# Kernel tuning notes

Measured on AMD Instinct MI355X. Metric: run time of the kernel, lower is better.

Reference implementation:

```python
import jax, jax.numpy as jnp
import numpy as np

B, L, DM = 4, 4096, 1024
DK, DV = 128, 128


def setup_inputs() -> dict:
    key = jax.random.key(0)
    kq, kk, kv, kwq, kwk, kwv = jax.random.split(key, 6)
    scale = 1.0 / np.sqrt(DM)
    return {
        "Q": jax.random.normal(kq, (B, L, DM), dtype=jnp.float32),
        "K": jax.random.normal(kk, (B, L, DM), dtype=jnp.float32),
        "V": jax.random.normal(kv, (B, L, DM), dtype=jnp.float32),
        "mask": jnp.ones((B, 1, L), dtype=jnp.int32),
        "WQ": jax.random.normal(kwq, (DM, DK), dtype=jnp.float32) * scale,
        "WK": jax.random.normal(kwk, (DM, DK), dtype=jnp.float32) * scale,
        "WV": jax.random.normal(kwv, (DM, DV), dtype=jnp.float32) * scale,
    }


def reference(Q, K, V, mask, WQ, WK, WV):
    # Projections (Dense, no bias): [B, L, dm] @ [dm, dk/dv]
    q = jnp.einsum("bld,dk->blk", Q, WQ)  # [B, L, dk]
    k = jnp.einsum("bld,dk->blk", K, WK)  # [B, L, dk]
    v = jnp.einsum("bld,dv->blv", V, WV)  # [B, L, dv]
    # Raw scores [B, L, L]
    qk = jnp.einsum("bqk,bsk->bqs", q, k)
    # Faithful to original: mask applied BEFORE scaling by 1/sqrt(dk)
    qk = jnp.where(mask == 1, qk, -jnp.inf)
    qk = qk / jnp.sqrt(jnp.asarray(DK, dtype=qk.dtype))
    attn = jax.nn.softmax(qk, axis=-1)
    return jnp.einsum("bqs,bsv->bqv", attn, v)  # [B, L, dv]
```

## Files before the change

### kernel.cpp

```cpp
#include <hip/hip_runtime.h>
#include <hip/hip_bf16.h>

#define B_  4
#define L_  4096
#define DM_ 1024
#define DK_ 128
#define DV_ 128
#define KS_ 4
#define ROWS_ (B_ * L_)

typedef __bf16 bf16x8 __attribute__((ext_vector_type(8)));
typedef float  f32x4  __attribute__((ext_vector_type(4)));

__device__ __forceinline__ void dma16(const void* g, void* l) {
    __builtin_amdgcn_global_load_lds(
        (const __attribute__((address_space(1))) void*)g,
        (__attribute__((address_space(3))) void*)l, 16, 0, 0);
}

#define WAITBAR0() __asm__ volatile("s_waitcnt vmcnt(0) lgkmcnt(0)\ns_barrier" ::: "memory")

__device__ __forceinline__ float rowmax_dpp(float v) {
    int x;
    x = __float_as_int(v);
    v = fmaxf(v, __int_as_float(__builtin_amdgcn_update_dpp(x, x, 0x121, 0xF, 0xF, false)));
    x = __float_as_int(v);
    v = fmaxf(v, __int_as_float(__builtin_amdgcn_update_dpp(x, x, 0x122, 0xF, 0xF, false)));
    x = __float_as_int(v);
    v = fmaxf(v, __int_as_float(__builtin_amdgcn_update_dpp(x, x, 0x124, 0xF, 0xF, false)));
    x = __float_as_int(v);
    v = fmaxf(v, __int_as_float(__builtin_amdgcn_update_dpp(x, x, 0x128, 0xF, 0xF, false)));
    return v;
}

__global__ __launch_bounds__(256) void wt_kernel(
    const float* __restrict__ WQ, const float* __restrict__ WK,
    const float* __restrict__ WV, __bf16* __restrict__ WT)
{
    const int mat = blockIdx.y;
    const float* W = (mat == 0) ? WQ : (mat == 1) ? WK : WV;
    const float scl = (mat == 0) ? 0.088388347648318447f : 1.0f;
    __bf16* Wt = WT + (size_t)mat * DK_ * DM_;

    __shared__ float lds[DK_][33];
    const int t  = threadIdx.x;
    const int d0 = blockIdx.x * 32;

    for (int i = 0; i < 16; ++i) {
        int idx = i * 256 + t;
        int dd = idx >> 7, n = idx & 127;
        lds[n][dd] = W[(size_t)(d0 + dd) * DK_ + n] * scl;
    }
    __syncthreads();
    for (int i = 0; i < 16; ++i) {
        int idx = i * 256 + t;
        int n = idx >> 5, dd = idx & 31;
        Wt[(size_t)n * DM_ + d0 + dd] = (__bf16)lds[n][dd];
    }
}

__global__ __launch_bounds__(256, 4) void proj_kernel(
    const float* __restrict__ Q, const float* __restrict__ K, const float* __restrict__ V,
    const __bf16* __restrict__ WT,
    __bf16* __restrict__ qb, __bf16* __restrict__ kb, __bf16* __restrict__ vT)
{
    const int mat = blockIdx.y;
    const float* X = (mat == 0) ? Q : (mat == 1) ? K : V;
    const __bf16* Wt = WT + (size_t)mat * DK_ * DM_;

    __shared__ __bf16 wbuf[2][128 * 64];

    const int t    = threadIdx.x;
    const int w    = t >> 6;
    const int l    = t & 63;
    const int quad = l >> 4;
    const int c16  = l & 15;
    const int m0   = blockIdx.x * 64 + w * 16;
    const float* xrow = &X[(size_t)(m0 + c16) * DM_];

    const __bf16* wg[4];
    for (int i = 0; i < 4; ++i) {
        int row = (w * 4 + i) * 8 + (l >> 3);
        int lc  = (l & 7) ^ (row & 7);
        wg[i] = Wt + (size_t)row * DM_ + lc * 8;
    }

    f32x4 acc[8];
    for (int i = 0; i < 8; ++i) acc[i] = {0.f, 0.f, 0.f, 0.f};

    for (int i = 0; i < 4; ++i)
        dma16(wg[i], &wbuf[0][(w * 4 + i) * 512]);
    float4 xn[4];
    for (int dd = 0; dd < 2; ++dd)
        for (int p = 0; p < 2; ++p)
            xn[dd * 2 + p] = *(const float4*)(xrow + dd * 32 + quad * 8 + p * 4);
    WAITBAR0();

    for (int kt = 0; kt < 16; ++kt) {
        const int cur = kt & 1, nxt = cur ^ 1;
        float4 xc[4];
        for (int i = 0; i < 4; ++i) xc[i] = xn[i];
        if (kt < 15) {
            const int d1 = (kt + 1) * 64;
            for (int i = 0; i < 4; ++i)
                dma16(wg[i] + d1, &wbuf[nxt][(w * 4 + i) * 512]);
            for (int dd = 0; dd < 2; ++dd)
                for (int p = 0; p < 2; ++p)
                    xn[dd * 2 + p] = *(const float4*)(xrow + d1 + dd * 32 + quad * 8 + p * 4);
        }

        for (int dd = 0; dd < 2; ++dd) {
            float4 x0 = xc[dd * 2], x1 = xc[dd * 2 + 1];
            bf16x8 af;
            af[0] = (__bf16)x0.x; af[1] = (__bf16)x0.y; af[2] = (__bf16)x0.z; af[3] = (__bf16)x0.w;
            af[4] = (__bf16)x1.x; af[5] = (__bf16)x1.y; af[6] = (__bf16)x1.z; af[7] = (__bf16)x1.w;
            for (int nt = 0; nt < 8; ++nt) {
                bf16x8 bfv = *(const bf16x8*)
                    &wbuf[cur][(nt * 16 + c16) * 64 + (((dd * 4 + quad) ^ (c16 & 7)) << 3)];
                acc[nt] = __builtin_amdgcn_mfma_f32_16x16x32_bf16(af, bfv, acc[nt], 0, 0, 0);
            }
        }
        if (kt < 15) WAITBAR0();
    }

    if (mat < 2) {
        __bf16* outp = (mat == 0) ? qb : kb;
        for (int nt = 0; nt < 8; ++nt)
            for (int r = 0; r < 4; ++r)
                outp[(size_t)(m0 + quad * 4 + r) * DK_ + nt * 16 + c16] = (__bf16)acc[nt][r];
    } else {
        for (int nt = 0; nt < 8; ++nt)
            for (int r = 0; r < 4; ++r) {
                int row = m0 + quad * 4 + r;
                int b = row >> 12, s = row & (L_ - 1);
                vT[((size_t)b * DV_ + nt * 16 + c16) * L_ + s] = (__bf16)acc[nt][r];
            }
    }
}

__global__ __launch_bounds__(256, 2) void attn_kernel(
    const __bf16* __restrict__ qb, const __bf16* __restrict__ kb,
    const __bf16* __restrict__ vT, const int* __restrict__ mask,
    __bf16* __restrict__ ob_part, float* __restrict__ ml_part)
{
    __shared__ __bf16 kbuf[2][64 * 128];
    __shared__ __bf16 vbuf[2][128 * 64];
    __shared__ __bf16 p_lds[4][16 * 76];

    const int t    = threadIdx.x;
    const int w    = t >> 6;
    const int l    = t & 63;
    const int quad = l >> 4;
    const int c16  = l & 15;

    const int combo = blockIdx.x & 15;
    const int b     = combo & 3;
    const int ks    = combo >> 2;
    const int qt    = blockIdx.x >> 4;
    const int m0    = qt * 64 + w * 16;
    const size_t bL = (size_t)b * L_;
    const int kbase = ks * (L_ / KS_);

    const __bf16* kg[4];
    const __bf16* vg[4];
    for (int i = 0; i < 4; ++i) {
        int kr  = (w * 4 + i) * 4 + (l >> 4);
        int klc = (l & 15) ^ (kr & 15);
        kg[i] = kb + (bL + kbase + kr) * DK_ + klc * 8;
        int vr  = (w * 4 + i) * 8 + (l >> 3);
        int vlc = (l & 7) ^ (vr & 7);
        vg[i] = vT + ((size_t)b * DV_ + vr) * L_ + kbase + vlc * 8;
    }

    bf16x8 qf[4];
    {
        const __bf16* qrow = &qb[(bL + m0 + c16) * DK_];
        for (int dt = 0; dt < 4; ++dt)
            qf[dt] = *(const bf16x8*)&qrow[dt * 32 + quad * 8];
    }

    unsigned int mbits = 0;
    for (int g = 0; g < 4; ++g) {
        const int4 mv = *(const int4*)&mask[bL + kbase + g * 256 + l * 4];
        bool ok = (mv.x == 1) && (mv.y == 1) && (mv.z == 1) && (mv.w == 1);
        unsigned long long bm = __ballot(ok);
        for (int cc = 0; cc < 4; ++cc)
            if (((bm >> (16 * cc)) & 0xFFFFull) == 0xFFFFull)
                mbits |= 1u << (g * 4 + cc);
    }

    bf16x8 onesv;
    for (int i = 0; i < 8; ++i) onesv[i] = (__bf16)1.0f;

    f32x4 o[8], osum;
    for (int i = 0; i < 8; ++i) o[i] = {0.f, 0.f, 0.f, 0.f};
    osum = {0.f, 0.f, 0.f, 0.f};
    float mst[4];
    for (int r = 0; r < 4; ++r) mst[r] = -1e30f;

    for (int i = 0; i < 4; ++i) dma16(kg[i], &kbuf[0][(w * 4 + i) * 512]);
    for (int i = 0; i < 4; ++i) dma16(vg[i], &vbuf[0][(w * 4 + i) * 512]);
    WAITBAR0();

    for (int sc = 0; sc < (L_ / KS_) / 64; ++sc) {
        const int cur = sc & 1, nxt = cur ^ 1;
        if (sc < 15) {
            for (int i = 0; i < 4; ++i)
                dma16(kg[i] + (size_t)(sc + 1) * 64 * DK_, &kbuf[nxt][(w * 4 + i) * 512]);
            for (int i = 0; i < 4; ++i)
                dma16(vg[i] + (sc + 1) * 64, &vbuf[nxt][(w * 4 + i) * 512]);
        }

        f32x4 sacc[4];
        for (int nt = 0; nt < 4; ++nt) sacc[nt] = {0.f, 0.f, 0.f, 0.f};
        for (int dt = 0; dt < 4; ++dt)
            for (int nt = 0; nt < 4; ++nt) {
                bf16x8 kf = *(const bf16x8*)
                    &kbuf[cur][(nt * 16 + c16) * 128 + (((dt * 4 + quad) ^ c16) << 3)];
                sacc[nt] = __builtin_amdgcn_mfma_f32_16x16x32_bf16(qf[dt], kf, sacc[nt], 0, 0, 0);
            }

        if (!((mbits >> sc) & 1)) {
            const int s0 = kbase + sc * 64;
            for (int nt = 0; nt < 4; ++nt) {
                int mk = mask[bL + s0 + nt * 16 + c16];
                for (int r = 0; r < 4; ++r)
                    if (mk != 1) sacc[nt][r] = -1e30f;
            }
        }

        float nm[4];
        bool up = false;
        for (int r = 0; r < 4; ++r) {
            float cm = fmaxf(fmaxf(sacc[0][r], sacc[1][r]), fmaxf(sacc[2][r], sacc[3][r]));
            cm = rowmax_dpp(cm);
            nm[r] = fmaxf(mst[r], cm);
            up |= (nm[r] > mst[r]);
        }
        if (__ballot(up)) {
            float alpha[4];
            for (int r = 0; r < 4; ++r) {
                alpha[r] = __expf(mst[r] - nm[r]);
                mst[r] = nm[r];
            }
            for (int vt = 0; vt < 8; ++vt)
                for (int r = 0; r < 4; ++r) o[vt][r] *= alpha[r];
            for (int r = 0; r < 4; ++r) osum[r] *= alpha[r];
        }

        for (int r = 0; r < 4; ++r)
            for (int nt = 0; nt < 4; ++nt) {
                float p = __expf(sacc[nt][r] - nm[r]);
                p_lds[w][(quad * 4 + r) * 76 + nt * 16 + c16] = (__bf16)p;
            }
        __asm__ volatile("s_waitcnt lgkmcnt(0)" ::: "memory");

        for (int kt = 0; kt < 2; ++kt) {
            bf16x8 pf = *(const bf16x8*)&p_lds[w][c16 * 76 + kt * 32 + quad * 8];
            for (int vt = 0; vt < 8; ++vt) {
                bf16x8 vf = *(const bf16x8*)
                    &vbuf[cur][(vt * 16 + c16) * 64 + (((kt * 4 + quad) ^ (c16 & 7)) << 3)];
                o[vt] = __builtin_amdgcn_mfma_f32_16x16x32_bf16(pf, vf, o[vt], 0, 0, 0);
            }
            osum = __builtin_amdgcn_mfma_f32_16x16x32_bf16(pf, onesv, osum, 0, 0, 0);
        }

        if (sc < 15) WAITBAR0();
    }

    __bf16* op = ob_part + ((size_t)ks * ROWS_ + bL + m0) * DV_;
    for (int vt = 0; vt < 8; ++vt)
        for (int r = 0; r < 4; ++r)
            op[(size_t)(quad * 4 + r) * DV_ + vt * 16 + c16] = (__bf16)o[vt][r];
    if (c16 == 0)
        for (int r = 0; r < 4; ++r) {
            size_t row = (size_t)ks * ROWS_ + bL + m0 + quad * 4 + r;
            ml_part[row * 2 + 0] = mst[r];
            ml_part[row * 2 + 1] = osum[r];
        }
}

__global__ __launch_bounds__(256) void combine_kernel(
    const __bf16* __restrict__ ob_part, const float* __restrict__ ml_part,
    float* __restrict__ out)
{
    const int gid = blockIdx.x * 256 + threadIdx.x;
    const int row = gid >> 5;
    const int c4  = (gid & 31) << 2;

    float m[KS_], lv[KS_];
    float M = -1e30f;
    for (int s = 0; s < KS_; ++s) {
        m[s]  = ml_part[((size_t)s * ROWS_ + row) * 2 + 0];
        lv[s] = ml_part[((size_t)s * ROWS_ + row) * 2 + 1];
        M = fmaxf(M, m[s]);
    }
    float Lt = 0.f, acc[4] = {0.f, 0.f, 0.f, 0.f};
    for (int s = 0; s < KS_; ++s) {
        float ws = __expf(m[s] - M);
        Lt += lv[s] * ws;
        const __bf16* op = ob_part + ((size_t)s * ROWS_ + row) * DV_ + c4;
        for (int c = 0; c < 4; ++c) acc[c] += (float)op[c] * ws;
    }
    float rL = 1.0f / Lt;
    for (int c = 0; c < 4; ++c)
        out[(size_t)row * DV_ + c4 + c] = acc[c] * rL;
}

extern "C" void kernel_launch(void* const* d_in, const int* in_sizes, int n_in,
                              void* d_out, int out_size, void* d_ws, size_t ws_size,
                              hipStream_t stream) {
    const float* Q    = (const float*)d_in[0];
    const float* K    = (const float*)d_in[1];
    const float* V    = (const float*)d_in[2];
    const int*   mask = (const int*)d_in[3];
    const float* WQ   = (const float*)d_in[4];
    const float* WK   = (const float*)d_in[5];
    const float* WV   = (const float*)d_in[6];
    float* out = (float*)d_out;

    __bf16* qb = (__bf16*)d_ws;
    __bf16* kb = qb + (size_t)ROWS_ * DK_;
    __bf16* vT = kb + (size_t)ROWS_ * DK_;
    __bf16* WT = vT + (size_t)ROWS_ * DV_;
    __bf16* ob_part = WT + (size_t)3 * DK_ * DM_;
    float*  ml_part = (float*)(ob_part + (size_t)KS_ * ROWS_ * DV_);

    wt_kernel<<<dim3(DM_ / 32, 3), 256, 0, stream>>>(WQ, WK, WV, WT);
    proj_kernel<<<dim3(ROWS_ / 64, 3), 256, 0, stream>>>(Q, K, V, WT, qb, kb, vT);
    attn_kernel<<<dim3((ROWS_ / 64) * KS_), 256, 0, stream>>>(qb, kb, vT, mask, ob_part, ml_part);
    combine_kernel<<<dim3(ROWS_ * 32 / 256), 256, 0, stream>>>(ob_part, ml_part, out);
}
```

Measured before the change: 289.6 us.

## Load projection weights directly into registers instead of LDS double-buffering

The projection kernel drops the LDS staging buffer and the per-step barriers for the weight tile. Each lane now loads its bf16 weight fragments straight from global memory into registers, double-buffered at half-tile granularity. The X prefetch depth grows to two K-steps and the loop is fully unrolled. Every wave now re-reads the weight rows from global/L2, which raises register pressure, so the occupancy hint drops from 4 to 3 blocks.

New measurement: 344.3 us. 18.9% more time.

```diff
diff --git a/kernel.cpp b/kernel.cpp
--- a/kernel.cpp
+++ b/kernel.cpp
@@ -59,7 +59,7 @@
     }
 }
 
-__global__ __launch_bounds__(256, 4) void proj_kernel(
+__global__ __launch_bounds__(256, 3) void proj_kernel(
     const float* __restrict__ Q, const float* __restrict__ K, const float* __restrict__ V,
     const __bf16* __restrict__ WT,
     __bf16* __restrict__ qb, __bf16* __restrict__ kb, __bf16* __restrict__ vT)
@@ -68,8 +68,6 @@
     const float* X = (mat == 0) ? Q : (mat == 1) ? K : V;
     const __bf16* Wt = WT + (size_t)mat * DK_ * DM_;
 
-    __shared__ __bf16 wbuf[2][128 * 64];
-
     const int t    = threadIdx.x;
     const int w    = t >> 6;
     const int l    = t & 63;
@@ -78,49 +76,50 @@
     const int m0   = blockIdx.x * 64 + w * 16;
     const float* xrow = &X[(size_t)(m0 + c16) * DM_];
 
-    const __bf16* wg[4];
-    for (int i = 0; i < 4; ++i) {
-        int row = (w * 4 + i) * 8 + (l >> 3);
-        int lc  = (l & 7) ^ (row & 7);
-        wg[i] = Wt + (size_t)row * DM_ + lc * 8;
-    }
+    const __bf16* wp[8];
+    for (int nt = 0; nt < 8; ++nt)
+        wp[nt] = Wt + (size_t)(nt * 16 + c16) * DM_ + quad * 8;
 
     f32x4 acc[8];
     for (int i = 0; i < 8; ++i) acc[i] = {0.f, 0.f, 0.f, 0.f};
 
-    for (int i = 0; i < 4; ++i)
-        dma16(wg[i], &wbuf[0][(w * 4 + i) * 512]);
-    float4 xn[4];
-    for (int dd = 0; dd < 2; ++dd)
-        for (int p = 0; p < 2; ++p)
-            xn[dd * 2 + p] = *(const float4*)(xrow + dd * 32 + quad * 8 + p * 4);
-    WAITBAR0();
-
+    bf16x8 wf[2][8];
+    float4 xn[2][4];
+
+    for (int nt = 0; nt < 8; ++nt)
+        wf[0][nt] = *(const bf16x8*)(wp[nt]);
+    for (int c = 0; c < 2; ++c)
+        for (int dd = 0; dd < 2; ++dd)
+            for (int p = 0; p < 2; ++p)
+                xn[c][dd * 2 + p] = *(const float4*)(xrow + c * 64 + dd * 32 + quad * 8 + p * 4);
+
+#pragma unroll
     for (int kt = 0; kt < 16; ++kt) {
-        const int cur = kt & 1, nxt = cur ^ 1;
         float4 xc[4];
-        for (int i = 0; i < 4; ++i) xc[i] = xn[i];
-        if (kt < 15) {
-            const int d1 = (kt + 1) * 64;
-            for (int i = 0; i < 4; ++i)
-                dma16(wg[i] + d1, &wbuf[nxt][(w * 4 + i) * 512]);
+        for (int i = 0; i < 4; ++i) xc[i] = xn[kt & 1][i];
+        if (kt < 14) {
+            const int d2 = (kt + 2) * 64;
             for (int dd = 0; dd < 2; ++dd)
                 for (int p = 0; p < 2; ++p)
-                    xn[dd * 2 + p] = *(const float4*)(xrow + d1 + dd * 32 + quad * 8 + p * 4);
+                    xn[kt & 1][dd * 2 + p] = *(const float4*)(xrow + d2 + dd * 32 + quad * 8 + p * 4);
         }
 
         for (int dd = 0; dd < 2; ++dd) {
+            if (dd == 0) {
+                for (int nt = 0; nt < 8; ++nt)
+                    wf[1][nt] = *(const bf16x8*)(wp[nt] + kt * 64 + 32);
+            } else if (kt < 15) {
+                for (int nt = 0; nt < 8; ++nt)
+                    wf[0][nt] = *(const bf16x8*)(wp[nt] + (kt + 1) * 64);
+            }
+
             float4 x0 = xc[dd * 2], x1 = xc[dd * 2 + 1];
             bf16x8 af;
             af[0] = (__bf16)x0.x; af[1] = (__bf16)x0.y; af[2] = (__bf16)x0.z; af[3] = (__bf16)x0.w;
             af[4] = (__bf16)x1.x; af[5] = (__bf16)x1.y; af[6] = (__bf16)x1.z; af[7] = (__bf16)x1.w;
-            for (int nt = 0; nt < 8; ++nt) {
-                bf16x8 bfv = *(const bf16x8*)
-                    &wbuf[cur][(nt * 16 + c16) * 64 + (((dd * 4 + quad) ^ (c16 & 7)) << 3)];
-                acc[nt] = __builtin_amdgcn_mfma_f32_16x16x32_bf16(af, bfv, acc[nt], 0, 0, 0);
-            }
-        }
-        if (kt < 15) WAITBAR0();
+            for (int nt = 0; nt < 8; ++nt)
+                acc[nt] = __builtin_amdgcn_mfma_f32_16x16x32_bf16(af, wf[dd][nt], acc[nt], 0, 0, 0);
+        }
     }
 
     if (mat < 2) {
```
